# Kernel optimization log

Hardware: AMD Instinct MI355X
Metric: run time of the kernel (lower is better)

Reference implementation:

```python
import jax, jax.numpy as jnp
import numpy as np

N_NODES = 100000

def graph_conv(x, src, dst, W_rel, W_root, b, num_nodes):
    # PyG GraphConv: out_i = lin_rel(sum_{j in N(i)} x_j) + lin_root(x_i)
    agg = jax.ops.segment_sum(x[src], dst, num_segments=num_nodes)  # [N, F_in]
    return agg @ W_rel + x @ W_root + b


def setup_inputs() -> dict:
    key = jax.random.key(0)
    ks = jax.random.split(key, 8)
    z = jax.random.normal(ks[0], (N_NODES, 64), dtype=jnp.float32)
    edge_index = jax.random.randint(ks[1], (2, 1600000), 0, N_NODES, dtype=jnp.int64)
    def glorot(k, fi, fo):
        s = (6.0 / (fi + fo)) ** 0.5
        return jax.random.uniform(k, (fi, fo), dtype=jnp.float32, minval=-s, maxval=s)
    return {
        "z": z,
        "edge_index": edge_index,
        "W_rel1": glorot(ks[2], 64, 32), "W_root1": glorot(ks[3], 64, 32), "b1": jnp.zeros((32,), jnp.float32),
        "W_rel2": glorot(ks[4], 32, 16), "W_root2": glorot(ks[5], 32, 16), "b2": jnp.zeros((16,), jnp.float32),
        "W_rel3": glorot(ks[6], 16, 2), "W_root3": glorot(ks[7], 16, 2), "b3": jnp.zeros((2,), jnp.float32),
    }


def reference(z, edge_index, W_rel1, W_root1, b1, W_rel2, W_root2, b2, W_rel3, W_root3, b3):
    src, dst = edge_index[0], edge_index[1]
    h = graph_conv(z, src, dst, W_rel1, W_root1, b1, N_NODES)
    h = jax.nn.relu(h)
    h = graph_conv(h, src, dst, W_rel2, W_root2, b2, N_NODES)
    h = jax.nn.relu(h)
    h = graph_conv(h, src, dst, W_rel3, W_root3, b3, N_NODES)
    return jax.nn.softmax(h, axis=-1)
```

## Files before the change

kernel.cpp:

```cpp
#include <hip/hip_runtime.h>


#define RNODES 128
#define NB_MAX 1024
#define CH 4096
#define CMAX 512

template <int Fin, int Fout, bool RELU>
__device__ __forceinline__ void lin_compute(const float* __restrict__ x,
                                            const float* __restrict__ W,
                                            int n, float* o) {
#pragma unroll
    for (int f = 0; f < Fout; ++f) o[f] = 0.f;
    const float* xr = x + (size_t)n * Fin;
#pragma unroll
    for (int k = 0; k < Fin; k += 4) {
        float4 v = *(const float4*)(xr + k);
        if (RELU) {
            v.x = fmaxf(v.x, 0.f); v.y = fmaxf(v.y, 0.f);
            v.z = fmaxf(v.z, 0.f); v.w = fmaxf(v.w, 0.f);
        }
        const float xv[4] = {v.x, v.y, v.z, v.w};
#pragma unroll
        for (int kk = 0; kk < 4; ++kk) {
            const float* wr = W + (size_t)(k + kk) * Fout;
#pragma unroll
            for (int f = 0; f < Fout; ++f)
                o[f] = fmaf(xv[kk], wr[f], o[f]);
        }
    }
}

template <int Fin, int Fout, bool RELU>
__global__ void linear_qg_kernel(const float* __restrict__ x,
                                 const float* __restrict__ Wrel,
                                 const float* __restrict__ Wroot,
                                 const float* __restrict__ bias,
                                 short* __restrict__ t,
                                 float* __restrict__ gscale,
                                 float* __restrict__ acc, int N) {
    int n = blockIdx.x * blockDim.x + threadIdx.x;
    const bool valid = (n < N);
    float o[Fout];

    if (blockIdx.y != 0) {
        if (!valid) return;
        lin_compute<Fin, Fout, RELU>(x, Wroot, n, o);
#pragma unroll
        for (int f = 0; f < Fout; ++f) o[f] += bias[f];
        float* arow = acc + (size_t)n * Fout;
        if constexpr (Fout >= 4) {
#pragma unroll
            for (int f = 0; f < Fout; f += 4)
                *(float4*)(arow + f) = make_float4(o[f], o[f+1], o[f+2], o[f+3]);
        } else {
            *(float2*)arow = make_float2(o[0], o[1]);
        }
        return;
    }

    float m = 0.f;
    if (valid) {
        lin_compute<Fin, Fout, RELU>(x, Wrel, n, o);
#pragma unroll
        for (int f = 0; f < Fout; ++f) m = fmaxf(m, fabsf(o[f]));
    }
    float wm = m;
#pragma unroll
    for (int off = 1; off < 64; off <<= 1)
        wm = fmaxf(wm, __shfl_xor(wm, off, 64));
    __shared__ float wmax[4];
    const int wv = threadIdx.x >> 6;
    if ((threadIdx.x & 63) == 0) wmax[wv] = wm;
    __syncthreads();
    const float g = fmaxf(wmax[wv & 2], wmax[(wv & 2) | 1]);
    if (!valid) return;
    const float inv = (g > 0.f) ? (32767.0f / g) : 0.f;
    if ((threadIdx.x & 127) == 0) gscale[n >> 7] = g * (1.0f / 32767.0f);

    short q[Fout];
#pragma unroll
    for (int f = 0; f < Fout; ++f) q[f] = (short)__float2int_rn(o[f] * inv);

    if constexpr (Fout == 32) {
        short* trow = t + (size_t)n * 32;
#pragma unroll
        for (int f = 0; f < 32; f += 8)
            *(int4*)(trow + f) = *(const int4*)(q + f);
    } else if constexpr (Fout == 16) {
        short* trow = t + (size_t)n * 16;
        *(int4*)(trow)     = *(const int4*)(q);
        *(int4*)(trow + 8) = *(const int4*)(q + 8);
    } else {
        ((int*)t)[n] = (int)(unsigned short)q[0] | ((int)q[1] << 16);
    }
}

__global__ void hist_chunked_kernel(const int* __restrict__ dst,
                                    int* __restrict__ chunkhist,
                                    int nE, int NB) {
    __shared__ int h[NB_MAX];
    const int c  = blockIdx.x;
    const int e0 = c * CH, e1 = min(e0 + CH, nE);
    for (int b = threadIdx.x; b < NB; b += blockDim.x) h[b] = 0;
    __syncthreads();
    for (int e = e0 + threadIdx.x; e < e1; e += blockDim.x)
        atomicAdd(&h[dst[e] >> 7], 1);
    __syncthreads();
    for (int b = threadIdx.x; b < NB; b += blockDim.x)
        chunkhist[(size_t)c * NB + b] = h[b];
}

__global__ void scan_chunkhist_kernel(int* __restrict__ chunkhist,
                                      int* __restrict__ gtotal,
                                      int C, int NB) {
    __shared__ int s[CMAX];
    const int b = blockIdx.x;
    const int t = threadIdx.x;
    int v = (t < C) ? chunkhist[(size_t)t * NB + b] : 0;
    s[t] = v;
    __syncthreads();
    for (int off = 1; off < CMAX; off <<= 1) {
        int u = (t >= off) ? s[t - off] : 0;
        __syncthreads();
        s[t] += u;
        __syncthreads();
    }
    if (t < C) chunkhist[(size_t)t * NB + b] = s[t] - v;
    if (t == CMAX - 1) gtotal[b] = s[t];
}

__global__ void scan_buckets_kernel(const int* __restrict__ gtotal,
                                    int* __restrict__ bptr, int NB, int nE) {
    __shared__ int s[NB_MAX];
    int t = threadIdx.x;
    int own = (t < NB) ? gtotal[t] : 0;
    s[t] = own;
    __syncthreads();
    for (int off = 1; off < NB_MAX; off <<= 1) {
        int v = (t >= off) ? s[t - off] : 0;
        __syncthreads();
        s[t] += v;
        __syncthreads();
    }
    if (t < NB) bptr[t] = s[t] - own;
    if (t == 0) bptr[NB] = nE;
}

__global__ void bucketize_det_kernel(const int* __restrict__ src,
                                     const int* __restrict__ dst,
                                     const int* __restrict__ chunkpre,
                                     const int* __restrict__ bptr,
                                     unsigned int* __restrict__ records,
                                     int nE, int NB) {
    __shared__ int lcur[NB_MAX];
    const int c  = blockIdx.x;
    const int e0 = c * CH, e1 = min(e0 + CH, nE);
    for (int b = threadIdx.x; b < NB; b += blockDim.x)
        lcur[b] = bptr[b] + chunkpre[(size_t)c * NB + b];
    __syncthreads();
    for (int e = e0 + threadIdx.x; e < e1; e += blockDim.x) {
        int d = dst[e];
        int b = d >> 7;
        int pos = atomicAdd(&lcur[b], 1);
        records[pos] = (unsigned int)src[e] | ((unsigned int)(d & 127) << 17);
    }
}

__global__ void place_merge_kernel(const unsigned int* __restrict__ records,
                                   const int* __restrict__ bptr,
                                   int* __restrict__ rowptr,
                                   int* __restrict__ srcs_sorted,
                                   int N, int nE, int NB) {
    __shared__ int hist[RNODES];
    __shared__ int s[RNODES];
    __shared__ int lcur[RNODES];
    const int b    = blockIdx.x;
    const int base = b * RNODES;
    const int nn   = min(RNODES, N - base);
    const int beg  = bptr[b], end = bptr[b + 1];
    const int t    = threadIdx.x;

    if (t < RNODES) hist[t] = 0;
    __syncthreads();
    for (int i = beg + t; i < end; i += blockDim.x)
        atomicAdd(&hist[records[i] >> 17], 1);
    __syncthreads();

    if (t < RNODES) s[t] = hist[t];
    __syncthreads();
    for (int off = 1; off < RNODES; off <<= 1) {
        int v = (t < RNODES && t >= off) ? s[t - off] : 0;
        __syncthreads();
        if (t < RNODES && t >= off) s[t] += v;
        __syncthreads();
    }
    if (t < nn) {
        int ex = beg + s[t] - hist[t];
        rowptr[base + t] = ex;
        lcur[t] = ex;
    }
    if (b == NB - 1 && t == 0) rowptr[N] = nE;
    __syncthreads();

    for (int i = beg + t; i < end; i += blockDim.x) {
        unsigned int rec = records[i];
        int pos = atomicAdd(&lcur[rec >> 17], 1);
        srcs_sorted[pos] = (int)(rec & 0x1FFFFu);
    }
}

__global__ void gather32_g_kernel(const short* __restrict__ t,
                                  const float* __restrict__ gscale,
                                  const int* __restrict__ rowptr,
                                  const int* __restrict__ srcs,
                                  const float* __restrict__ rootacc,
                                  float* __restrict__ out, int N) {
    int tid = blockIdx.x * blockDim.x + threadIdx.x;
    int n  = tid >> 4;
    int fp = tid & 15;
    if (n >= N) return;

    const int* tp = (const int*)t;
    int beg = rowptr[n], end = rowptr[n + 1];
    float sx = 0.f, sy = 0.f;
    int e = beg;
    for (; e + 8 <= end; e += 8) {
        int s[8];
#pragma unroll
        for (int u = 0; u < 8; ++u) s[u] = srcs[e + u];
        int q[8]; float sc[8];
#pragma unroll
        for (int u = 0; u < 8; ++u) {
            q[u]  = tp[(size_t)s[u] * 16 + fp];
            sc[u] = gscale[s[u] >> 7];
        }
#pragma unroll
        for (int u = 0; u < 8; ++u) {
            sx = fmaf(sc[u], (float)((short)(q[u] & 0xFFFF)), sx);
            sy = fmaf(sc[u], (float)(q[u] >> 16), sy);
        }
    }
    for (; e < end; ++e) {
        int s0 = srcs[e];
        int qv = tp[(size_t)s0 * 16 + fp];
        float sc = gscale[s0 >> 7];
        sx = fmaf(sc, (float)((short)(qv & 0xFFFF)), sx);
        sy = fmaf(sc, (float)(qv >> 16), sy);
    }

    const float2 r0 = *(const float2*)(rootacc + (size_t)n * 32 + 2 * fp);
    *(float2*)(out + (size_t)n * 32 + 2 * fp) = make_float2(r0.x + sx, r0.y + sy);
}

__global__ void gather16_g_kernel(const short* __restrict__ t,
                                  const float* __restrict__ gscale,
                                  const int* __restrict__ rowptr,
                                  const int* __restrict__ srcs,
                                  const float* __restrict__ rootacc,
                                  float* __restrict__ out, int N) {
    int tid = blockIdx.x * blockDim.x + threadIdx.x;
    int n  = tid >> 3;
    int fp = tid & 7;
    if (n >= N) return;

    const int* tp = (const int*)t;
    int beg = rowptr[n], end = rowptr[n + 1];
    float sx = 0.f, sy = 0.f;
    int e = beg;
    for (; e + 8 <= end; e += 8) {
        int s[8];
#pragma unroll
        for (int u = 0; u < 8; ++u) s[u] = srcs[e + u];
        int q[8]; float sc[8];
#pragma unroll
        for (int u = 0; u < 8; ++u) {
            q[u]  = tp[(size_t)s[u] * 8 + fp];
            sc[u] = gscale[s[u] >> 7];
        }
#pragma unroll
        for (int u = 0; u < 8; ++u) {
            sx = fmaf(sc[u], (float)((short)(q[u] & 0xFFFF)), sx);
            sy = fmaf(sc[u], (float)(q[u] >> 16), sy);
        }
    }
    for (; e < end; ++e) {
        int s0 = srcs[e];
        int qv = tp[(size_t)s0 * 8 + fp];
        float sc = gscale[s0 >> 7];
        sx = fmaf(sc, (float)((short)(qv & 0xFFFF)), sx);
        sy = fmaf(sc, (float)(qv >> 16), sy);
    }

    const float2 r0 = *(const float2*)(rootacc + (size_t)n * 16 + 2 * fp);
    *(float2*)(out + (size_t)n * 16 + 2 * fp) = make_float2(r0.x + sx, r0.y + sy);
}

__global__ void gather2_g_kernel(const short* __restrict__ t,
                                 const float* __restrict__ gscale,
                                 const int* __restrict__ rowptr,
                                 const int* __restrict__ srcs,
                                 const float* __restrict__ rootacc,
                                 float* __restrict__ out, int N) {
    int tid = blockIdx.x * blockDim.x + threadIdx.x;
    int n  = tid >> 2;
    int fp = tid & 3;
    if (n >= N) return;

    const int* tp = (const int*)t;
    int beg = rowptr[n], end = rowptr[n + 1];
    float sx = 0.f, sy = 0.f;
    int e = beg + fp;
    for (; e + 12 < end; e += 16) {
        int s0 = srcs[e], s1 = srcs[e + 4], s2 = srcs[e + 8], s3 = srcs[e + 12];
        int r0 = tp[s0], r1 = tp[s1], r2 = tp[s2], r3 = tp[s3];
        float c0 = gscale[s0 >> 7], c1 = gscale[s1 >> 7];
        float c2 = gscale[s2 >> 7], c3 = gscale[s3 >> 7];
        sx = fmaf(c0, (float)((short)(r0 & 0xFFFF)), sx);
        sy = fmaf(c0, (float)(r0 >> 16), sy);
        sx = fmaf(c1, (float)((short)(r1 & 0xFFFF)), sx);
        sy = fmaf(c1, (float)(r1 >> 16), sy);
        sx = fmaf(c2, (float)((short)(r2 & 0xFFFF)), sx);
        sy = fmaf(c2, (float)(r2 >> 16), sy);
        sx = fmaf(c3, (float)((short)(r3 & 0xFFFF)), sx);
        sy = fmaf(c3, (float)(r3 >> 16), sy);
    }
    for (; e < end; e += 4) {
        int s0 = srcs[e];
        int r = tp[s0];
        float c = gscale[s0 >> 7];
        sx = fmaf(c, (float)((short)(r & 0xFFFF)), sx);
        sy = fmaf(c, (float)(r >> 16), sy);
    }
    sx += __shfl_xor(sx, 1, 64); sy += __shfl_xor(sy, 1, 64);
    sx += __shfl_xor(sx, 2, 64); sy += __shfl_xor(sy, 2, 64);

    if (fp == 0) {
        const float2 r0 = *(const float2*)(rootacc + (size_t)n * 2);
        float a = r0.x + sx, b = r0.y + sy;
        float m = fmaxf(a, b);
        float ea = __expf(a - m), eb = __expf(b - m);
        float inv = 1.0f / (ea + eb);
        *(float2*)(out + (size_t)n * 2) = make_float2(ea * inv, eb * inv);
    }
}

template <int Fin, int Fout, bool RELU>
__global__ void linear2_kernel(const float* __restrict__ x,
                               const float* __restrict__ Wrel,
                               const float* __restrict__ Wroot,
                               const float* __restrict__ bias,
                               float* __restrict__ t,
                               float* __restrict__ acc, int N) {
    const bool rootTask = (blockIdx.y != 0);
    const float* __restrict__ W = rootTask ? Wroot : Wrel;
    float* __restrict__ outp    = rootTask ? acc : t;

    int n = blockIdx.x * blockDim.x + threadIdx.x;
    if (n >= N) return;

    float o[Fout];
    lin_compute<Fin, Fout, RELU>(x, W, n, o);
    if (rootTask) {
#pragma unroll
        for (int f = 0; f < Fout; ++f) o[f] += bias[f];
    }
    float* op = outp + (size_t)n * Fout;
    if constexpr (Fout >= 4) {
#pragma unroll
        for (int f = 0; f < Fout; f += 4)
            *(float4*)(op + f) = make_float4(o[f], o[f + 1], o[f + 2], o[f + 3]);
    } else {
        *(float2*)op = make_float2(o[0], o[1]);
    }
}

template <int F>
__global__ void scatter_kernel(const float* __restrict__ t,
                               const int* __restrict__ src,
                               const int* __restrict__ dst,
                               float* __restrict__ acc, int nE) {
    int tid = blockIdx.x * blockDim.x + threadIdx.x;
    int e = tid / F;
    if (e >= nE) return;
    int f = tid & (F - 1);
    atomicAdd(acc + (long)dst[e] * F + f, t[(long)src[e] * F + f]);
}

__global__ void softmax2_kernel(const float* __restrict__ h, float* __restrict__ out, int N) {
    int n = blockIdx.x * blockDim.x + threadIdx.x;
    if (n >= N) return;
    float a = h[2 * n], b = h[2 * n + 1];
    float m = fmaxf(a, b);
    float ea = __expf(a - m), eb = __expf(b - m);
    float inv = 1.0f / (ea + eb);
    out[2 * n] = ea * inv;
    out[2 * n + 1] = eb * inv;
}

extern "C" void kernel_launch(void* const* d_in, const int* in_sizes, int n_in,
                              void* d_out, int out_size, void* d_ws, size_t ws_size,
                              hipStream_t stream) {
    const float* z      = (const float*)d_in[0];
    const int*   ei     = (const int*)d_in[1];
    const float* Wrel1  = (const float*)d_in[2];
    const float* Wroot1 = (const float*)d_in[3];
    const float* b1     = (const float*)d_in[4];
    const float* Wrel2  = (const float*)d_in[5];
    const float* Wroot2 = (const float*)d_in[6];
    const float* b2     = (const float*)d_in[7];
    const float* Wrel3  = (const float*)d_in[8];
    const float* Wroot3 = (const float*)d_in[9];
    const float* b3     = (const float*)d_in[10];

    const int N  = in_sizes[0] / 64;
    const int nE = in_sizes[1] / 2;
    const int* src = ei;
    const int* dst = ei + nE;
    const int NB = (N + RNODES - 1) / RNODES;
    const int C  = (nE + CH - 1) / CH;

    char* wsb = (char*)d_ws;
    size_t off = 0;
    auto take = [&](size_t bytes) -> void* {
        void* p = (void*)(wsb + off);
        off = (off + bytes + 255) & ~(size_t)255;
        return p;
    };
    int*          chunkhist   = (int*)take((size_t)CMAX * NB_MAX * 4);
    int*          gtotal      = (int*)take((size_t)NB_MAX * 4);
    int*          bptr        = (int*)take((size_t)(NB_MAX + 1) * 4);
    unsigned int* records     = (unsigned int*)take((size_t)nE * 4);
    int*          rowptr      = (int*)take((size_t)(N + 1) * 4);
    int*          srcs_sorted = (int*)take((size_t)nE * 4);
    short*        t1          = (short*)take((size_t)N * 32 * 2);
    float*        gs1         = (float*)take((size_t)NB_MAX * 4);
    float*        h1          = (float*)take((size_t)N * 32 * 4);
    short*        t2          = (short*)take((size_t)N * 16 * 2);
    float*        gs2         = (float*)take((size_t)NB_MAX * 4);
    float*        h2          = (float*)take((size_t)N * 16 * 4);
    short*        t3          = (short*)take((size_t)N * 2 * 2);
    float*        gs3         = (float*)take((size_t)NB_MAX * 4);
    float*        h3          = (float*)take((size_t)N * 2 * 4);
    const size_t needed = off;

    const int B = 256;
    const int nodeBlocks = (N + B - 1) / B;
    const dim3 linGrid(nodeBlocks, 2);
    const bool packOK = (N <= (1 << 17)) && (NB <= NB_MAX) && (C <= CMAX);

    if (ws_size >= needed && packOK) {
        hist_chunked_kernel<<<C, 512, 0, stream>>>(dst, chunkhist, nE, NB);
        scan_chunkhist_kernel<<<NB, CMAX, 0, stream>>>(chunkhist, gtotal, C, NB);
        scan_buckets_kernel<<<1, NB_MAX, 0, stream>>>(gtotal, bptr, NB, nE);
        bucketize_det_kernel<<<C, 512, 0, stream>>>(src, dst, chunkhist, bptr, records, nE, NB);
        place_merge_kernel<<<NB, 512, 0, stream>>>(records, bptr, rowptr, srcs_sorted, N, nE, NB);

        linear_qg_kernel<64, 32, false><<<linGrid, B, 0, stream>>>(
            z, Wrel1, Wroot1, b1, t1, gs1, h1, N);
        gather32_g_kernel<<<((size_t)N * 16 + B - 1) / B, B, 0, stream>>>(
            t1, gs1, rowptr, srcs_sorted, h1, h1, N);

        linear_qg_kernel<32, 16, true><<<linGrid, B, 0, stream>>>(
            h1, Wrel2, Wroot2, b2, t2, gs2, h2, N);
        gather16_g_kernel<<<((size_t)N * 8 + B - 1) / B, B, 0, stream>>>(
            t2, gs2, rowptr, srcs_sorted, h2, h2, N);

        linear_qg_kernel<16, 2, true><<<linGrid, B, 0, stream>>>(
            h2, Wrel3, Wroot3, b3, t3, gs3, h3, N);
        gather2_g_kernel<<<((size_t)N * 4 + B - 1) / B, B, 0, stream>>>(
            t3, gs3, rowptr, srcs_sorted, h3, (float*)d_out, N);
    } else {
        float* regionA = (float*)d_ws;
        float* regionB = regionA + (size_t)N * 32;
        float* ft1 = regionA;
        float* fh1 = regionB;
        float* ft2 = regionA;
        float* fh2 = regionA + (size_t)N * 16;
        float* ft3 = regionB;
        float* fh3 = regionB + (size_t)N * 2;
        linear2_kernel<64, 32, false><<<linGrid, B, 0, stream>>>(z, Wrel1, Wroot1, b1, ft1, fh1, N);
        scatter_kernel<32><<<((size_t)nE * 32 + B - 1) / B, B, 0, stream>>>(ft1, src, dst, fh1, nE);
        linear2_kernel<32, 16, true><<<linGrid, B, 0, stream>>>(fh1, Wrel2, Wroot2, b2, ft2, fh2, N);
        scatter_kernel<16><<<((size_t)nE * 16 + B - 1) / B, B, 0, stream>>>(ft2, src, dst, fh2, nE);
        linear2_kernel<16, 2, true><<<linGrid, B, 0, stream>>>(fh2, Wrel3, Wroot3, b3, ft3, fh3, N);
        scatter_kernel<2><<<((size_t)nE * 2 + B - 1) / B, B, 0, stream>>>(ft3, src, dst, fh3, nE);
        softmax2_kernel<<<nodeBlocks, B, 0, stream>>>(fh3, (float*)d_out, N);
    }
}
```

Measured before the change: 234.7 us.

## Fuse layer-2/3 linear transforms into preceding gather kernels

Merges each neighbor-gather kernel with the following layer's relu+linear+int16 quantization, computing the small matvec via cross-lane shuffle reductions within the node's lane group. This removes two kernel launches and the write/readback of the full fp32 hidden activations between gather and linear. Quantization scale groups change to per-block (32 or 64 nodes), so gather indexing shifts accordingly; it adds many shuffles and register pressure per thread. linear_qg_kernel is simplified to only the 64->32 instance.

New measurement: 270.4 us. 1.15x slower.

```diff
diff --git a/kernel.cpp b/kernel.cpp
--- a/kernel.cpp
+++ b/kernel.cpp
@@ -49,13 +49,9 @@
 #pragma unroll
         for (int f = 0; f < Fout; ++f) o[f] += bias[f];
         float* arow = acc + (size_t)n * Fout;
-        if constexpr (Fout >= 4) {
-#pragma unroll
-            for (int f = 0; f < Fout; f += 4)
-                *(float4*)(arow + f) = make_float4(o[f], o[f+1], o[f+2], o[f+3]);
-        } else {
-            *(float2*)arow = make_float2(o[0], o[1]);
-        }
+#pragma unroll
+        for (int f = 0; f < Fout; f += 4)
+            *(float4*)(arow + f) = make_float4(o[f], o[f+1], o[f+2], o[f+3]);
         return;
     }
 
@@ -81,19 +77,10 @@
     short q[Fout];
 #pragma unroll
     for (int f = 0; f < Fout; ++f) q[f] = (short)__float2int_rn(o[f] * inv);
-
-    if constexpr (Fout == 32) {
-        short* trow = t + (size_t)n * 32;
-#pragma unroll
-        for (int f = 0; f < 32; f += 8)
-            *(int4*)(trow + f) = *(const int4*)(q + f);
-    } else if constexpr (Fout == 16) {
-        short* trow = t + (size_t)n * 16;
-        *(int4*)(trow)     = *(const int4*)(q);
-        *(int4*)(trow + 8) = *(const int4*)(q + 8);
-    } else {
-        ((int*)t)[n] = (int)(unsigned short)q[0] | ((int)q[1] << 16);
-    }
+    short* trow = t + (size_t)n * 32;
+#pragma unroll
+    for (int f = 0; f < 32; f += 8)
+        *(int4*)(trow + f) = *(const int4*)(q + f);
 }
 
 __global__ void hist_chunked_kernel(const int* __restrict__ dst,
@@ -210,90 +197,182 @@
     }
 }
 
-__global__ void gather32_g_kernel(const short* __restrict__ t,
-                                  const float* __restrict__ gscale,
-                                  const int* __restrict__ rowptr,
-                                  const int* __restrict__ srcs,
-                                  const float* __restrict__ rootacc,
-                                  float* __restrict__ out, int N) {
-    int tid = blockIdx.x * blockDim.x + threadIdx.x;
-    int n  = tid >> 4;
-    int fp = tid & 15;
-    if (n >= N) return;
-
-    const int* tp = (const int*)t;
-    int beg = rowptr[n], end = rowptr[n + 1];
+__global__ void g32_lin2_kernel(const short* __restrict__ t1,
+                                const float* __restrict__ gs1,
+                                const int* __restrict__ rowptr,
+                                const int* __restrict__ srcs,
+                                const float* __restrict__ h1root,
+                                const float* __restrict__ Wrel2,
+                                const float* __restrict__ Wroot2,
+                                const float* __restrict__ b2,
+                                short* __restrict__ t2,
+                                float* __restrict__ gs2,
+                                float* __restrict__ h2root,
+                                int N) {
+    const int tid = threadIdx.x;
+    const int fp  = tid & 15;
+    const int n   = blockIdx.x * 32 + (tid >> 4);
+    const bool valid = (n < N);
+
     float sx = 0.f, sy = 0.f;
-    int e = beg;
-    for (; e + 8 <= end; e += 8) {
-        int s[8];
-#pragma unroll
-        for (int u = 0; u < 8; ++u) s[u] = srcs[e + u];
-        int q[8]; float sc[8];
-#pragma unroll
-        for (int u = 0; u < 8; ++u) {
-            q[u]  = tp[(size_t)s[u] * 16 + fp];
-            sc[u] = gscale[s[u] >> 7];
-        }
-#pragma unroll
-        for (int u = 0; u < 8; ++u) {
-            sx = fmaf(sc[u], (float)((short)(q[u] & 0xFFFF)), sx);
-            sy = fmaf(sc[u], (float)(q[u] >> 16), sy);
-        }
-    }
-    for (; e < end; ++e) {
-        int s0 = srcs[e];
-        int qv = tp[(size_t)s0 * 16 + fp];
-        float sc = gscale[s0 >> 7];
-        sx = fmaf(sc, (float)((short)(qv & 0xFFFF)), sx);
-        sy = fmaf(sc, (float)(qv >> 16), sy);
-    }
-
-    const float2 r0 = *(const float2*)(rootacc + (size_t)n * 32 + 2 * fp);
-    *(float2*)(out + (size_t)n * 32 + 2 * fp) = make_float2(r0.x + sx, r0.y + sy);
-}
-
-__global__ void gather16_g_kernel(const short* __restrict__ t,
-                                  const float* __restrict__ gscale,
-                                  const int* __restrict__ rowptr,
-                                  const int* __restrict__ srcs,
-                                  const float* __restrict__ rootacc,
-                                  float* __restrict__ out, int N) {
-    int tid = blockIdx.x * blockDim.x + threadIdx.x;
-    int n  = tid >> 3;
-    int fp = tid & 7;
-    if (n >= N) return;
-
-    const int* tp = (const int*)t;
-    int beg = rowptr[n], end = rowptr[n + 1];
+    if (valid) {
+        const int* tp = (const int*)t1;
+        int beg = rowptr[n], end = rowptr[n + 1];
+        int e = beg;
+        for (; e + 8 <= end; e += 8) {
+            int s[8];
+#pragma unroll
+            for (int u = 0; u < 8; ++u) s[u] = srcs[e + u];
+            int q[8]; float sc[8];
+#pragma unroll
+            for (int u = 0; u < 8; ++u) {
+                q[u]  = tp[(size_t)s[u] * 16 + fp];
+                sc[u] = gs1[s[u] >> 7];
+            }
+#pragma unroll
+            for (int u = 0; u < 8; ++u) {
+                sx = fmaf(sc[u], (float)((short)(q[u] & 0xFFFF)), sx);
+                sy = fmaf(sc[u], (float)(q[u] >> 16), sy);
+            }
+        }
+        for (; e < end; ++e) {
+            int s0 = srcs[e];
+            int qv = tp[(size_t)s0 * 16 + fp];
+            float sc = gs1[s0 >> 7];
+            sx = fmaf(sc, (float)((short)(qv & 0xFFFF)), sx);
+            sy = fmaf(sc, (float)(qv >> 16), sy);
+        }
+        const float2 r0 = *(const float2*)(h1root + (size_t)n * 32 + 2 * fp);
+        sx += r0.x; sy += r0.y;
+    }
+
+    const float a0 = fmaxf(sx, 0.f), a1 = fmaxf(sy, 0.f);
+    float prel[16], prot[16];
+    {
+        const float* w0 = Wrel2  + (size_t)(2 * fp) * 16;
+        const float* w1 = Wrel2  + (size_t)(2 * fp + 1) * 16;
+        const float* v0 = Wroot2 + (size_t)(2 * fp) * 16;
+        const float* v1 = Wroot2 + (size_t)(2 * fp + 1) * 16;
+#pragma unroll
+        for (int j = 0; j < 16; ++j) {
+            prel[j] = a0 * w0[j] + a1 * w1[j];
+            prot[j] = a0 * v0[j] + a1 * v1[j];
+        }
+    }
+#pragma unroll
+    for (int off = 1; off < 16; off <<= 1) {
+#pragma unroll
+        for (int j = 0; j < 16; ++j) {
+            prel[j] += __shfl_xor(prel[j], off, 64);
+            prot[j] += __shfl_xor(prot[j], off, 64);
+        }
+    }
+
+    float m = 0.f;
+#pragma unroll
+    for (int j = 0; j < 16; ++j) m = fmaxf(m, fabsf(prel[j]));
+    m = fmaxf(m, __shfl_xor(m, 16, 64));
+    m = fmaxf(m, __shfl_xor(m, 32, 64));
+    __shared__ float wmax[8];
+    if ((tid & 63) == 0) wmax[tid >> 6] = m;
+    __syncthreads();
+    float g = wmax[0];
+#pragma unroll
+    for (int w = 1; w < 8; ++w) g = fmaxf(g, wmax[w]);
+    const float inv = (g > 0.f) ? (32767.0f / g) : 0.f;
+    if (tid == 0) gs2[blockIdx.x] = g * (1.0f / 32767.0f);
+
+    if (!valid || fp >= 8) return;
+    short2 qq;
+    qq.x = (short)__float2int_rn(prel[2 * fp]     * inv);
+    qq.y = (short)__float2int_rn(prel[2 * fp + 1] * inv);
+    ((short2*)(t2 + (size_t)n * 16))[fp] = qq;
+    float2 hh;
+    hh.x = prot[2 * fp]     + b2[2 * fp];
+    hh.y = prot[2 * fp + 1] + b2[2 * fp + 1];
+    ((float2*)(h2root + (size_t)n * 16))[fp] = hh;
+}
+
+__global__ void g16_lin3_kernel(const short* __restrict__ t2,
+                                const float* __restrict__ gs2,
+                                const int* __restrict__ rowptr,
+                                const int* __restrict__ srcs,
+                                const float* __restrict__ h2root,
+                                const float* __restrict__ Wrel3,
+                                const float* __restrict__ Wroot3,
+                                const float* __restrict__ b3,
+                                short* __restrict__ t3,
+                                float* __restrict__ gs3,
+                                float* __restrict__ h3root,
+                                int N) {
+    const int tid = threadIdx.x;
+    const int fp  = tid & 7;
+    const int n   = blockIdx.x * 64 + (tid >> 3);
+    const bool valid = (n < N);
+
     float sx = 0.f, sy = 0.f;
-    int e = beg;
-    for (; e + 8 <= end; e += 8) {
-        int s[8];
-#pragma unroll
-        for (int u = 0; u < 8; ++u) s[u] = srcs[e + u];
-        int q[8]; float sc[8];
-#pragma unroll
-        for (int u = 0; u < 8; ++u) {
-            q[u]  = tp[(size_t)s[u] * 8 + fp];
-            sc[u] = gscale[s[u] >> 7];
-        }
-#pragma unroll
-        for (int u = 0; u < 8; ++u) {
-            sx = fmaf(sc[u], (float)((short)(q[u] & 0xFFFF)), sx);
-            sy = fmaf(sc[u], (float)(q[u] >> 16), sy);
-        }
-    }
-    for (; e < end; ++e) {
-        int s0 = srcs[e];
-        int qv = tp[(size_t)s0 * 8 + fp];
-        float sc = gscale[s0 >> 7];
-        sx = fmaf(sc, (float)((short)(qv & 0xFFFF)), sx);
-        sy = fmaf(sc, (float)(qv >> 16), sy);
-    }
-
-    const float2 r0 = *(const float2*)(rootacc + (size_t)n * 16 + 2 * fp);
-    *(float2*)(out + (size_t)n * 16 + 2 * fp) = make_float2(r0.x + sx, r0.y + sy);
+    if (valid) {
+        const int* tp = (const int*)t2;
+        int beg = rowptr[n], end = rowptr[n + 1];
+        int e = beg;
+        for (; e + 8 <= end; e += 8) {
+            int s[8];
+#pragma unroll
+            for (int u = 0; u < 8; ++u) s[u] = srcs[e + u];
+            int q[8]; float sc[8];
+#pragma unroll
+            for (int u = 0; u < 8; ++u) {
+                q[u]  = tp[(size_t)s[u] * 8 + fp];
+                sc[u] = gs2[s[u] >> 5];
+            }
+#pragma unroll
+            for (int u = 0; u < 8; ++u) {
+                sx = fmaf(sc[u], (float)((short)(q[u] & 0xFFFF)), sx);
+                sy = fmaf(sc[u], (float)(q[u] >> 16), sy);
+            }
+        }
+        for (; e < end; ++e) {
+            int s0 = srcs[e];
+            int qv = tp[(size_t)s0 * 8 + fp];
+            float sc = gs2[s0 >> 5];
+            sx = fmaf(sc, (float)((short)(qv & 0xFFFF)), sx);
+            sy = fmaf(sc, (float)(qv >> 16), sy);
+        }
+        const float2 r0 = *(const float2*)(h2root + (size_t)n * 16 + 2 * fp);
+        sx += r0.x; sy += r0.y;
+    }
+
+    const float a0 = fmaxf(sx, 0.f), a1 = fmaxf(sy, 0.f);
+    float pr0 = a0 * Wrel3[(2 * fp) * 2]     + a1 * Wrel3[(2 * fp + 1) * 2];
+    float pr1 = a0 * Wrel3[(2 * fp) * 2 + 1] + a1 * Wrel3[(2 * fp + 1) * 2 + 1];
+    float po0 = a0 * Wroot3[(2 * fp) * 2]     + a1 * Wroot3[(2 * fp + 1) * 2];
+    float po1 = a0 * Wroot3[(2 * fp) * 2 + 1] + a1 * Wroot3[(2 * fp + 1) * 2 + 1];
+#pragma unroll
+    for (int off = 1; off < 8; off <<= 1) {
+        pr0 += __shfl_xor(pr0, off, 64);
+        pr1 += __shfl_xor(pr1, off, 64);
+        po0 += __shfl_xor(po0, off, 64);
+        po1 += __shfl_xor(po1, off, 64);
+    }
+
+    float m = fmaxf(fabsf(pr0), fabsf(pr1));
+    m = fmaxf(m, __shfl_xor(m, 8, 64));
+    m = fmaxf(m, __shfl_xor(m, 16, 64));
+    m = fmaxf(m, __shfl_xor(m, 32, 64));
+    __shared__ float wmax[8];
+    if ((tid & 63) == 0) wmax[tid >> 6] = m;
+    __syncthreads();
+    float g = wmax[0];
+#pragma unroll
+    for (int w = 1; w < 8; ++w) g = fmaxf(g, wmax[w]);
+    const float inv = (g > 0.f) ? (32767.0f / g) : 0.f;
+    if (tid == 0) gs3[blockIdx.x] = g * (1.0f / 32767.0f);
+
+    if (!valid || fp != 0) return;
+    int qx = (int)(unsigned short)(short)__float2int_rn(pr0 * inv)
+           | ((int)(short)__float2int_rn(pr1 * inv) << 16);
+    ((int*)t3)[n] = qx;
+    *(float2*)(h3root + (size_t)n * 2) = make_float2(po0 + b3[0], po1 + b3[1]);
 }
 
 __global__ void gather2_g_kernel(const short* __restrict__ t,
@@ -314,8 +393,8 @@
     for (; e + 12 < end; e += 16) {
         int s0 = srcs[e], s1 = srcs[e + 4], s2 = srcs[e + 8], s3 = srcs[e + 12];
         int r0 = tp[s0], r1 = tp[s1], r2 = tp[s2], r3 = tp[s3];
-        float c0 = gscale[s0 >> 7], c1 = gscale[s1 >> 7];
-        float c2 = gscale[s2 >> 7], c3 = gscale[s3 >> 7];
+        float c0 = gscale[s0 >> 6], c1 = gscale[s1 >> 6];
+        float c2 = gscale[s2 >> 6], c3 = gscale[s3 >> 6];
         sx = fmaf(c0, (float)((short)(r0 & 0xFFFF)), sx);
         sy = fmaf(c0, (float)(r0 >> 16), sy);
         sx = fmaf(c1, (float)((short)(r1 & 0xFFFF)), sx);
@@ -328,7 +407,7 @@
     for (; e < end; e += 4) {
         int s0 = srcs[e];
         int r = tp[s0];
-        float c = gscale[s0 >> 7];
+        float c = gscale[s0 >> 6];
         sx = fmaf(c, (float)((short)(r & 0xFFFF)), sx);
         sy = fmaf(c, (float)(r >> 16), sy);
     }
@@ -419,6 +498,8 @@
     const int* dst = ei + nE;
     const int NB = (N + RNODES - 1) / RNODES;
     const int C  = (nE + CH - 1) / CH;
+    const int G32 = (N + 31) / 32;
+    const int G64 = (N + 63) / 64;
 
     char* wsb = (char*)d_ws;
     size_t off = 0;
@@ -437,10 +518,10 @@
     float*        gs1         = (float*)take((size_t)NB_MAX * 4);
     float*        h1          = (float*)take((size_t)N * 32 * 4);
     short*        t2          = (short*)take((size_t)N * 16 * 2);
-    float*        gs2         = (float*)take((size_t)NB_MAX * 4);
+    float*        gs2         = (float*)take((size_t)G32 * 4);
     float*        h2          = (float*)take((size_t)N * 16 * 4);
     short*        t3          = (short*)take((size_t)N * 2 * 2);
-    float*        gs3         = (float*)take((size_t)NB_MAX * 4);
+    float*        gs3         = (float*)take((size_t)G64 * 4);
     float*        h3          = (float*)take((size_t)N * 2 * 4);
     const size_t needed = off;
 
@@ -458,16 +539,13 @@
 
         linear_qg_kernel<64, 32, false><<<linGrid, B, 0, stream>>>(
             z, Wrel1, Wroot1, b1, t1, gs1, h1, N);
-        gather32_g_kernel<<<((size_t)N * 16 + B - 1) / B, B, 0, stream>>>(
-            t1, gs1, rowptr, srcs_sorted, h1, h1, N);
-
-        linear_qg_kernel<32, 16, true><<<linGrid, B, 0, stream>>>(
-            h1, Wrel2, Wroot2, b2, t2, gs2, h2, N);
-        gather16_g_kernel<<<((size_t)N * 8 + B - 1) / B, B, 0, stream>>>(
-            t2, gs2, rowptr, srcs_sorted, h2, h2, N);
-
-        linear_qg_kernel<16, 2, true><<<linGrid, B, 0, stream>>>(
-            h2, Wrel3, Wroot3, b3, t3, gs3, h3, N);
+
+        g32_lin2_kernel<<<G32, 512, 0, stream>>>(
+            t1, gs1, rowptr, srcs_sorted, h1, Wrel2, Wroot2, b2, t2, gs2, h2, N);
+
+        g16_lin3_kernel<<<G64, 512, 0, stream>>>(
+            t2, gs2, rowptr, srcs_sorted, h2, Wrel3, Wroot3, b3, t3, gs3, h3, N);
+
         gather2_g_kernel<<<((size_t)N * 4 + B - 1) / B, B, 0, stream>>>(
             t3, gs3, rowptr, srcs_sorted, h3, (float*)d_out, N);
     } else {
```

## Fuse layer-1 gather with layer-2 linear and int16 quantization

Applied to the files above, without the earlier changes.

Merges the layer-1 neighbor gather with the layer-2 ReLU, dense transform and quantization into one kernel of 32 nodes per 512-thread block. The aggregated rows stay in shared memory instead of round-tripping h1 through global memory, and one kernel launch is removed. Quantization scale groups shrink from 128 to 32 nodes, so the layer-2 gather now indexes scales by s>>5. The trade-off is a block-level reduction with two syncthreads per 32 nodes and more shared memory per block, which may lower occupancy for the memory-bound gather.

Result: slower. 259.6 us (+10.6%).

```diff
diff --git a/kernel.cpp b/kernel.cpp
--- a/kernel.cpp
+++ b/kernel.cpp
@@ -210,47 +210,89 @@
     }
 }
 
-__global__ void gather32_g_kernel(const short* __restrict__ t,
-                                  const float* __restrict__ gscale,
-                                  const int* __restrict__ rowptr,
-                                  const int* __restrict__ srcs,
-                                  const float* __restrict__ rootacc,
-                                  float* __restrict__ out, int N) {
-    int tid = blockIdx.x * blockDim.x + threadIdx.x;
-    int n  = tid >> 4;
-    int fp = tid & 15;
-    if (n >= N) return;
-
-    const int* tp = (const int*)t;
-    int beg = rowptr[n], end = rowptr[n + 1];
+__global__ void g32lin2_kernel(const short* __restrict__ t1,
+                               const float* __restrict__ gs1,
+                               const int* __restrict__ rowptr,
+                               const int* __restrict__ srcs,
+                               const float* __restrict__ h1root,
+                               const float* __restrict__ Wrel2,
+                               const float* __restrict__ Wroot2,
+                               const float* __restrict__ b2,
+                               short* __restrict__ t2,
+                               float* __restrict__ gs2,
+                               float* __restrict__ h2root,
+                               int N) {
+    __shared__ float accs[32 * 34];
+    __shared__ float Wr[512], Wo[512];
+    __shared__ float wmax[8];
+    const int tid = threadIdx.x;
+    Wr[tid] = Wrel2[tid];
+    Wo[tid] = Wroot2[tid];
+
+    const int nl = tid >> 4;
+    const int fp = tid & 15;
+    const int n  = blockIdx.x * 32 + nl;
+    const bool valid = (n < N);
+
     float sx = 0.f, sy = 0.f;
-    int e = beg;
-    for (; e + 8 <= end; e += 8) {
-        int s[8];
-#pragma unroll
-        for (int u = 0; u < 8; ++u) s[u] = srcs[e + u];
-        int q[8]; float sc[8];
-#pragma unroll
-        for (int u = 0; u < 8; ++u) {
-            q[u]  = tp[(size_t)s[u] * 16 + fp];
-            sc[u] = gscale[s[u] >> 7];
-        }
-#pragma unroll
-        for (int u = 0; u < 8; ++u) {
-            sx = fmaf(sc[u], (float)((short)(q[u] & 0xFFFF)), sx);
-            sy = fmaf(sc[u], (float)(q[u] >> 16), sy);
-        }
-    }
-    for (; e < end; ++e) {
-        int s0 = srcs[e];
-        int qv = tp[(size_t)s0 * 16 + fp];
-        float sc = gscale[s0 >> 7];
-        sx = fmaf(sc, (float)((short)(qv & 0xFFFF)), sx);
-        sy = fmaf(sc, (float)(qv >> 16), sy);
-    }
-
-    const float2 r0 = *(const float2*)(rootacc + (size_t)n * 32 + 2 * fp);
-    *(float2*)(out + (size_t)n * 32 + 2 * fp) = make_float2(r0.x + sx, r0.y + sy);
+    if (valid) {
+        const int* tp = (const int*)t1;
+        int beg = rowptr[n], end = rowptr[n + 1];
+        int e = beg;
+        for (; e + 8 <= end; e += 8) {
+            int s[8];
+#pragma unroll
+            for (int u = 0; u < 8; ++u) s[u] = srcs[e + u];
+            int q[8]; float sc[8];
+#pragma unroll
+            for (int u = 0; u < 8; ++u) {
+                q[u]  = tp[(size_t)s[u] * 16 + fp];
+                sc[u] = gs1[s[u] >> 7];
+            }
+#pragma unroll
+            for (int u = 0; u < 8; ++u) {
+                sx = fmaf(sc[u], (float)((short)(q[u] & 0xFFFF)), sx);
+                sy = fmaf(sc[u], (float)(q[u] >> 16), sy);
+            }
+        }
+        for (; e < end; ++e) {
+            int s0 = srcs[e];
+            int qv = tp[(size_t)s0 * 16 + fp];
+            float sc = gs1[s0 >> 7];
+            sx = fmaf(sc, (float)((short)(qv & 0xFFFF)), sx);
+            sy = fmaf(sc, (float)(qv >> 16), sy);
+        }
+        const float2 r0 = *(const float2*)(h1root + (size_t)n * 32 + 2 * fp);
+        sx += r0.x; sy += r0.y;
+    }
+    accs[nl * 34 + 2 * fp]     = valid ? fmaxf(sx, 0.f) : 0.f;
+    accs[nl * 34 + 2 * fp + 1] = valid ? fmaxf(sy, 0.f) : 0.f;
+    __syncthreads();
+
+    float orel = 0.f, oroot = 0.f;
+    const float* arow = accs + nl * 34;
+#pragma unroll
+    for (int k = 0; k < 32; ++k) {
+        const float a = arow[k];
+        orel  = fmaf(a, Wr[k * 16 + fp], orel);
+        oroot = fmaf(a, Wo[k * 16 + fp], oroot);
+    }
+
+    float m = fabsf(orel);
+#pragma unroll
+    for (int off = 1; off < 64; off <<= 1)
+        m = fmaxf(m, __shfl_xor(m, off, 64));
+    if ((tid & 63) == 0) wmax[tid >> 6] = m;
+    __syncthreads();
+    float g = wmax[0];
+#pragma unroll
+    for (int w = 1; w < 8; ++w) g = fmaxf(g, wmax[w]);
+    const float inv = (g > 0.f) ? (32767.0f / g) : 0.f;
+    if (tid == 0) gs2[blockIdx.x] = g * (1.0f / 32767.0f);
+
+    if (!valid) return;
+    t2[(size_t)n * 16 + fp] = (short)__float2int_rn(orel * inv);
+    h2root[(size_t)n * 16 + fp] = oroot + b2[fp];
 }
 
 __global__ void gather16_g_kernel(const short* __restrict__ t,
@@ -276,7 +318,7 @@
 #pragma unroll
         for (int u = 0; u < 8; ++u) {
             q[u]  = tp[(size_t)s[u] * 8 + fp];
-            sc[u] = gscale[s[u] >> 7];
+            sc[u] = gscale[s[u] >> 5];
         }
 #pragma unroll
         for (int u = 0; u < 8; ++u) {
@@ -287,7 +329,7 @@
     for (; e < end; ++e) {
         int s0 = srcs[e];
         int qv = tp[(size_t)s0 * 8 + fp];
-        float sc = gscale[s0 >> 7];
+        float sc = gscale[s0 >> 5];
         sx = fmaf(sc, (float)((short)(qv & 0xFFFF)), sx);
         sy = fmaf(sc, (float)(qv >> 16), sy);
     }
@@ -419,6 +461,7 @@
     const int* dst = ei + nE;
     const int NB = (N + RNODES - 1) / RNODES;
     const int C  = (nE + CH - 1) / CH;
+    const int G32 = (N + 31) / 32;
 
     char* wsb = (char*)d_ws;
     size_t off = 0;
@@ -437,7 +480,7 @@
     float*        gs1         = (float*)take((size_t)NB_MAX * 4);
     float*        h1          = (float*)take((size_t)N * 32 * 4);
     short*        t2          = (short*)take((size_t)N * 16 * 2);
-    float*        gs2         = (float*)take((size_t)NB_MAX * 4);
+    float*        gs2         = (float*)take((size_t)G32 * 4);
     float*        h2          = (float*)take((size_t)N * 16 * 4);
     short*        t3          = (short*)take((size_t)N * 2 * 2);
     float*        gs3         = (float*)take((size_t)NB_MAX * 4);
@@ -458,11 +501,10 @@
 
         linear_qg_kernel<64, 32, false><<<linGrid, B, 0, stream>>>(
             z, Wrel1, Wroot1, b1, t1, gs1, h1, N);
-        gather32_g_kernel<<<((size_t)N * 16 + B - 1) / B, B, 0, stream>>>(
-            t1, gs1, rowptr, srcs_sorted, h1, h1, N);
-
-        linear_qg_kernel<32, 16, true><<<linGrid, B, 0, stream>>>(
-            h1, Wrel2, Wroot2, b2, t2, gs2, h2, N);
+
+        g32lin2_kernel<<<G32, 512, 0, stream>>>(
+            t1, gs1, rowptr, srcs_sorted, h1, Wrel2, Wroot2, b2, t2, gs2, h2, N);
+
         gather16_g_kernel<<<((size_t)N * 8 + B - 1) / B, B, 0, stream>>>(
             t2, gs2, rowptr, srcs_sorted, h2, h2, N);
 
```
